# Kernel tuning notes

Hardware: AMD Instinct MI355X
Metric: run time of the kernel (lower is better)

The kernel has to match this reference:

```python
import jax, jax.numpy as jnp
import numpy as np

N_NODES = 100000
N_EDGES = 1600000
F_IN = 128
HID = 128
N_CLS = 7


def _sage_conv(x, src, dst, Wl, bl, Wr, n_nodes, deg_inv):
    # mean-aggregate neighbor messages at destination nodes
    msg = x[src]                                            # [E, d] gather
    agg = jax.ops.segment_sum(msg, dst, num_segments=n_nodes)
    agg = agg * deg_inv[:, None]                            # mean
    # PyG SAGEConv: lin_l(aggr) + lin_r(x); bias only on lin_l
    return agg @ Wl.T + bl + x @ Wr.T


def setup_inputs() -> dict:
    key = jax.random.key(0)
    ks = jax.random.split(key, 12)
    x = jax.random.normal(ks[0], (N_NODES, F_IN), dtype=jnp.float32)
    edge_index = jax.random.randint(ks[1], (2, N_EDGES), 0, N_NODES, dtype=jnp.int32)
    s = 0.05
    return {
        "x": x,
        "edge_index": edge_index,
        "W1l": jax.random.normal(ks[2], (HID, F_IN), dtype=jnp.float32) * s,
        "b1": jax.random.normal(ks[3], (HID,), dtype=jnp.float32) * s,
        "W1r": jax.random.normal(ks[4], (HID, F_IN), dtype=jnp.float32) * s,
        "W2l": jax.random.normal(ks[5], (HID, HID), dtype=jnp.float32) * s,
        "b2": jax.random.normal(ks[6], (HID,), dtype=jnp.float32) * s,
        "W2r": jax.random.normal(ks[7], (HID, HID), dtype=jnp.float32) * s,
        "W3l": jax.random.normal(ks[8], (N_CLS, HID), dtype=jnp.float32) * s,
        "b3": jax.random.normal(ks[9], (N_CLS,), dtype=jnp.float32) * s,
        "W3r": jax.random.normal(ks[10], (N_CLS, HID), dtype=jnp.float32) * s,
    }


def reference(x, edge_index, W1l, b1, W1r, W2l, b2, W2r, W3l, b3, W3r):
    src, dst = edge_index[0], edge_index[1]
    n = x.shape[0]
    # in-degree for mean aggregation (shared by all layers)
    deg = jax.ops.segment_sum(jnp.ones((src.shape[0],), x.dtype), dst, num_segments=n)
    deg_inv = jnp.where(deg > 0, 1.0 / deg, 0.0)

    h = _sage_conv(x, src, dst, W1l, b1, W1r, n, deg_inv)
    h = jax.nn.relu(h)  # dropout is identity in eval mode
    h = _sage_conv(h, src, dst, W2l, b2, W2r, n, deg_inv)
    h = jax.nn.relu(h)
    h = _sage_conv(h, src, dst, W3l, b3, W3r, n, deg_inv)
    return jax.nn.log_softmax(h, axis=1)
```

## Files before the change

kernel.cpp:

```cpp
#include <hip/hip_runtime.h>
#include <hip/hip_bf16.h>

#define NFEAT 128

typedef __attribute__((ext_vector_type(8))) short frag8;
typedef __attribute__((ext_vector_type(4))) float f32x4;

__device__ __forceinline__ unsigned short f2bf(float f) {
  unsigned int u = __builtin_bit_cast(unsigned int, f);
  u += 0x7fffu + ((u >> 16) & 1u);
  return (unsigned short)(u >> 16);
}
__device__ __forceinline__ unsigned int pack2(float lo, float hi) {
  return (unsigned int)f2bf(lo) | ((unsigned int)f2bf(hi) << 16);
}
__device__ __forceinline__ void acc_pair(float* acc, unsigned int u) {
  acc[0] += __builtin_bit_cast(float, u << 16);
  acc[1] += __builtin_bit_cast(float, u);
}
__device__ __forceinline__ void acc_uint4(float* a, const uint4& f) {
  acc_pair(a + 0, f.x);
  acc_pair(a + 2, f.y);
  acc_pair(a + 4, f.z);
  acc_pair(a + 6, f.w);
}

__global__ __launch_bounds__(256) void k_bucket_count(
    const int* __restrict__ dst, int* __restrict__ bucket_cnt, int E, int NB, int chunk) {
  __shared__ int hist[512];
  int t = threadIdx.x;
  hist[t] = 0;
  hist[t + 256] = 0;
  __syncthreads();
  int beg = blockIdx.x * chunk, end = min(beg + chunk, E);
  for (int i = beg + t; i < end; i += 256) atomicAdd(&hist[dst[i] >> 8], 1);
  __syncthreads();
  for (int k = t; k < NB; k += 256)
    if (hist[k]) atomicAdd(&bucket_cnt[k], hist[k]);
}

__global__ void k_bucket_scan(const int* __restrict__ bucket_cnt,
                              int* __restrict__ bucket_base,
                              int* __restrict__ bucket_cursor, int NB, int E) {
  __shared__ int sm[512];
  int t = threadIdx.x;
  int v = (t < NB) ? bucket_cnt[t] : 0;
  sm[t] = v;
  __syncthreads();
  for (int off = 1; off < 512; off <<= 1) {
    int add = (t >= off) ? sm[t - off] : 0;
    __syncthreads();
    sm[t] += add;
    __syncthreads();
  }
  int excl = sm[t] - v;
  if (t < NB) {
    bucket_base[t] = excl;
    bucket_cursor[t] = excl;
  }
  if (t == 0) bucket_base[NB] = E;
}

__global__ __launch_bounds__(256) void k_bucket_fill(
    const int* __restrict__ src, const int* __restrict__ dst,
    int* __restrict__ bucket_cursor, unsigned int* __restrict__ tmp,
    int E, int NB, int chunk) {
  __shared__ int hist[512];
  __shared__ int cur[512];
  int t = threadIdx.x;
  hist[t] = 0;
  hist[t + 256] = 0;
  __syncthreads();
  int beg = blockIdx.x * chunk, end = min(beg + chunk, E);
  for (int i = beg + t; i < end; i += 256) atomicAdd(&hist[dst[i] >> 8], 1);
  __syncthreads();
  for (int k = t; k < 512; k += 256)
    cur[k] = (k < NB && hist[k]) ? atomicAdd(&bucket_cursor[k], hist[k]) : 0;
  __syncthreads();
  for (int i = beg + t; i < end; i += 256) {
    int d = dst[i];
    int p = atomicAdd(&cur[d >> 8], 1);
    tmp[p] = (((unsigned int)(d & 255)) << 24) | (unsigned int)src[i];
  }
}

__global__ __launch_bounds__(256) void k_local_sort(
    const unsigned int* __restrict__ tmp, const int* __restrict__ bucket_base,
    int* __restrict__ csr, int* __restrict__ row_ptr, float* __restrict__ dinv,
    int N, int E) {
  __shared__ int cnt[256];
  __shared__ int scan_s[256];
  int b = blockIdx.x, t = threadIdx.x;
  int base = bucket_base[b];
  int cnt_b = bucket_base[b + 1] - base;
  cnt[t] = 0;
  __syncthreads();
  for (int i = t; i < cnt_b; i += 256) atomicAdd(&cnt[tmp[base + i] >> 24], 1);
  __syncthreads();
  int v = cnt[t];
  scan_s[t] = v;
  __syncthreads();
  for (int off = 1; off < 256; off <<= 1) {
    int add = (t >= off) ? scan_s[t - off] : 0;
    __syncthreads();
    scan_s[t] += add;
    __syncthreads();
  }
  int excl = scan_s[t] - v;
  int node = b * 256 + t;
  if (node <= N) row_ptr[node] = base + excl;
  if (node < N) dinv[node] = (v > 0) ? (1.0f / (float)v) : 0.0f;
  __syncthreads();
  cnt[t] = base + excl;
  __syncthreads();
  for (int i = t; i < cnt_b; i += 256) {
    unsigned int u = tmp[base + i];
    int q = atomicAdd(&cnt[u >> 24], 1);
    csr[q] = (int)(u & 0x00FFFFFFu);
  }
}

__global__ __launch_bounds__(256) void k_setup(
    const float* __restrict__ w1l, const float* __restrict__ w1r,
    const float* __restrict__ w2l, const float* __restrict__ w2r,
    const float* __restrict__ W3l, const float* __restrict__ W3r,
    unsigned short* __restrict__ Wbf, unsigned short* __restrict__ Wc,
    const float* __restrict__ x, unsigned int* __restrict__ Xbf,
    int n_pairs, int* __restrict__ bucket_cnt, int do_x) {
  int gid = blockIdx.x * 256 + threadIdx.x;
  int gstride = gridDim.x * 256;
  if (gid < 512) bucket_cnt[gid] = 0;
  if (gid < 65536) {
    int m = gid >> 14, off = gid & 16383;
    const float* srcw = (m == 0) ? w1l : (m == 1) ? w1r : (m == 2) ? w2l : w2r;
    Wbf[gid] = f2bf(srcw[off]);
  }
  if (gid < 2048) {
    int r = gid >> 7, c = gid & 127;
    float v = 0.f;
    if (r < 7) v = W3l[r * NFEAT + c];
    else if (r >= 8 && r < 15) v = W3r[(r - 8) * NFEAT + c];
    Wc[gid] = f2bf(v);
  }
  if (do_x) {
    for (int i = gid; i < n_pairs; i += gstride) {
      float2 v = *(const float2*)(x + (size_t)i * 2);
      Xbf[i] = pack2(v.x, v.y);
    }
  }
}

__global__ __launch_bounds__(256) void k_aggregate(
    const unsigned int* __restrict__ xp, const int* __restrict__ row_ptr,
    const int* __restrict__ csr, const float* __restrict__ dinv,
    unsigned int* __restrict__ Aout, int n) {
  int wv = threadIdx.x >> 6, lane = threadIdx.x & 63;
  int v = blockIdx.x * 4 + wv;
  if (v >= n) return;
  int beg = row_ptr[v], end = row_ptr[v + 1];
  float dv = dinv[v];
  int slot = lane >> 4, part = lane & 15;

  int idx = 0;
  if (beg + lane < end) idx = csr[beg + lane];

  float acc[8] = {0.f, 0.f, 0.f, 0.f, 0.f, 0.f, 0.f, 0.f};
  for (int j = beg; j < end; j += 16) {
    int sidx[4];
#pragma unroll
    for (int b = 0; b < 4; ++b) {
      int rel = (j - beg) + b * 4 + slot;
      sidx[b] = __shfl(idx, rel & 63);
    }
    uint4 f[4];
#pragma unroll
    for (int b = 0; b < 4; ++b) {
      f[b] = make_uint4(0u, 0u, 0u, 0u);
      int e = j + b * 4 + slot;
      if (e < end) {
        int rel = e - beg;
        int s = (rel < 64) ? sidx[b] : csr[e];
        f[b] = *(const uint4*)(xp + (size_t)s * (NFEAT / 2) + part * 4);
      }
    }
#pragma unroll
    for (int b = 0; b < 4; ++b) acc_uint4(acc, f[b]);
  }
#pragma unroll
  for (int k = 0; k < 8; ++k) {
    acc[k] += __shfl_xor(acc[k], 16);
    acc[k] += __shfl_xor(acc[k], 32);
  }
  if (slot == 0) {
    uint4 o;
    o.x = pack2(acc[0] * dv, acc[1] * dv);
    o.y = pack2(acc[2] * dv, acc[3] * dv);
    o.z = pack2(acc[4] * dv, acc[5] * dv);
    o.w = pack2(acc[6] * dv, acc[7] * dv);
    *(uint4*)(Aout + (size_t)v * (NFEAT / 2) + part * 4) = o;
  }
}

__global__ __launch_bounds__(256) void k_aggregate_f32(
    const float* __restrict__ xp, const int* __restrict__ row_ptr,
    const int* __restrict__ csr, const float* __restrict__ dinv,
    unsigned int* __restrict__ Aout, int n) {
  int wv = threadIdx.x >> 6, lane = threadIdx.x & 63;
  int v = blockIdx.x * 4 + wv;
  if (v >= n) return;
  int beg = row_ptr[v], end = row_ptr[v + 1];
  float dv = dinv[v];
  int slot = lane >> 5;
  int part = lane & 31;
  float acc[4] = {0.f, 0.f, 0.f, 0.f};
  for (int j = beg; j < end; j += 16) {
    float4 f[8];
#pragma unroll
    for (int b = 0; b < 8; ++b) {
      f[b] = make_float4(0.f, 0.f, 0.f, 0.f);
      int e = j + b * 2 + slot;
      if (e < end) {
        int si = csr[e];
        f[b] = *(const float4*)(xp + (size_t)si * NFEAT + part * 4);
      }
    }
#pragma unroll
    for (int b = 0; b < 8; ++b) {
      acc[0] += f[b].x; acc[1] += f[b].y; acc[2] += f[b].z; acc[3] += f[b].w;
    }
  }
#pragma unroll
  for (int k = 0; k < 4; ++k) acc[k] += __shfl_xor(acc[k], 32);
  if (slot == 0) {
    uint2 o;
    o.x = pack2(acc[0] * dv, acc[1] * dv);
    o.y = pack2(acc[2] * dv, acc[3] * dv);
    *(uint2*)(Aout + (size_t)v * (NFEAT / 2) + part * 2) = o;
  }
}

template <bool X_IS_F32, bool INPLACE>
__global__ __launch_bounds__(256, 4) void k_gemm(
    const unsigned short* __restrict__ A, const void* __restrict__ X,
    const unsigned short* __restrict__ Wl, const unsigned short* __restrict__ Wr,
    const float* __restrict__ bias, unsigned short* __restrict__ Out,
    int M, int ntiles) {
  int wv = threadIdx.x >> 6, lane = threadIdx.x & 63;
  int lr = lane & 15, kq = lane >> 4;
  int kb0 = kq * 8;

  frag8 wl[2][4], wr[2][4];
  float bias_c[2];
#pragma unroll
  for (int ci = 0; ci < 2; ++ci) {
    int wrow = (wv * 2 + ci) * 16 + lr;
    bias_c[ci] = bias[wrow];
#pragma unroll
    for (int kk = 0; kk < 4; ++kk) {
      wl[ci][kk] = *(const frag8*)(Wl + (size_t)wrow * NFEAT + kk * 32 + kb0);
      wr[ci][kk] = *(const frag8*)(Wr + (size_t)wrow * NFEAT + kk * 32 + kb0);
    }
  }

  for (int tile = blockIdx.x; tile < ntiles; tile += gridDim.x) {
    int m0 = tile * 16;
    int row = m0 + lr;
    bool rowok = row < M;
    frag8 aA[4], aX[4];
#pragma unroll
    for (int kk = 0; kk < 4; ++kk) {
      aA[kk] = frag8{};
      aX[kk] = frag8{};
      if (rowok) {
        aA[kk] = *(const frag8*)(A + (size_t)row * NFEAT + kk * 32 + kb0);
        if constexpr (X_IS_F32) {
          const float* xp = (const float*)X + (size_t)row * NFEAT + kk * 32 + kb0;
          float4 v0 = *(const float4*)xp;
          float4 v1 = *(const float4*)(xp + 4);
          frag8 a;
          a[0] = (short)f2bf(v0.x); a[1] = (short)f2bf(v0.y);
          a[2] = (short)f2bf(v0.z); a[3] = (short)f2bf(v0.w);
          a[4] = (short)f2bf(v1.x); a[5] = (short)f2bf(v1.y);
          a[6] = (short)f2bf(v1.z); a[7] = (short)f2bf(v1.w);
          aX[kk] = a;
        } else {
          aX[kk] = *(const frag8*)((const unsigned short*)X + (size_t)row * NFEAT + kk * 32 + kb0);
        }
      }
    }
    if constexpr (INPLACE) __syncthreads();
    f32x4 acc[2] = {};
#pragma unroll
    for (int kk = 0; kk < 4; ++kk) {
#pragma unroll
      for (int ci = 0; ci < 2; ++ci) {
        acc[ci] = __builtin_amdgcn_mfma_f32_16x16x32_bf16(aA[kk], wl[ci][kk], acc[ci], 0, 0, 0);
        acc[ci] = __builtin_amdgcn_mfma_f32_16x16x32_bf16(aX[kk], wr[ci][kk], acc[ci], 0, 0, 0);
      }
    }
#pragma unroll
    for (int ci = 0; ci < 2; ++ci) {
#pragma unroll
      for (int r = 0; r < 4; ++r) {
        int orow = m0 + kq * 4 + r;
        if (orow < M) {
          int ocol = (wv * 2 + ci) * 16 + lr;
          float val = acc[ci][r] + bias_c[ci];
          Out[(size_t)orow * NFEAT + ocol] = f2bf(fmaxf(val, 0.f));
        }
      }
    }
  }
}

__global__ __launch_bounds__(256) void k_proj7m(
    const unsigned short* __restrict__ H, const unsigned short* __restrict__ Wc,
    float* __restrict__ P, float* __restrict__ Q, int M, int ntiles) {
  int wv = threadIdx.x >> 6, lane = threadIdx.x & 63;
  int lr = lane & 15, kq = lane >> 4;
  int kb0 = kq * 8;
  frag8 wb[4];
#pragma unroll
  for (int kk = 0; kk < 4; ++kk)
    wb[kk] = *(const frag8*)(Wc + (size_t)lr * NFEAT + kk * 32 + kb0);

  int tile = blockIdx.x * 4 + wv;
  if (tile >= ntiles) return;
  int m0 = tile * 16;
  int row = m0 + lr;
  bool rowok = row < M;
  frag8 a[4];
#pragma unroll
  for (int kk = 0; kk < 4; ++kk) {
    a[kk] = frag8{};
    if (rowok) a[kk] = *(const frag8*)(H + (size_t)row * NFEAT + kk * 32 + kb0);
  }
  f32x4 acc = {};
#pragma unroll
  for (int kk = 0; kk < 4; ++kk)
    acc = __builtin_amdgcn_mfma_f32_16x16x32_bf16(a[kk], wb[kk], acc, 0, 0, 0);
#pragma unroll
  for (int r = 0; r < 4; ++r) {
    int orow = m0 + kq * 4 + r;
    if (orow < M) {
      if (lr < 8) P[(size_t)orow * 8 + lr] = acc[r];
      else Q[(size_t)orow * 8 + (lr - 8)] = acc[r];
    }
  }
}

__global__ __launch_bounds__(256) void k_layer3s(
    const float* __restrict__ P, const float* __restrict__ Q,
    const int* __restrict__ row_ptr, const int* __restrict__ csr,
    const float* __restrict__ dinv, const float* __restrict__ b3,
    float* __restrict__ out, int n) {
  int wv = threadIdx.x >> 6, lane = threadIdx.x & 63;
  int v = blockIdx.x * 4 + wv;
  if (v >= n) return;
  int beg = row_ptr[v], end = row_ptr[v + 1];
  int g = lane >> 3, c = lane & 7;
  float acc = 0.f;
  for (int j = beg; j < end; j += 16) {
    float f0 = 0.f, f1 = 0.f;
    int e0 = j + g, e1 = j + 8 + g;
    if (e0 < end) f0 = P[(size_t)csr[e0] * 8 + c];
    if (e1 < end) f1 = P[(size_t)csr[e1] * 8 + c];
    acc += f0 + f1;
  }
  acc += __shfl_xor(acc, 8);
  acc += __shfl_xor(acc, 16);
  acc += __shfl_xor(acc, 32);
  float z_own = acc * dinv[v] + Q[(size_t)v * 8 + c] + ((c < 7) ? b3[c] : 0.f);
  float mx = -1e30f, se = 0.f;
  float zz[7];
#pragma unroll
  for (int cc = 0; cc < 7; ++cc) {
    zz[cc] = __shfl(z_own, cc);
    mx = fmaxf(mx, zz[cc]);
  }
#pragma unroll
  for (int cc = 0; cc < 7; ++cc) se += __expf(zz[cc] - mx);
  float lse = mx + __logf(se);
  if (lane < 7) out[(size_t)v * 7 + lane] = z_own - lse;
}

extern "C" void kernel_launch(void* const* d_in, const int* in_sizes, int n_in,
                              void* d_out, int out_size, void* d_ws, size_t ws_size,
                              hipStream_t stream) {
  const float* x = (const float*)d_in[0];
  const int* ei = (const int*)d_in[1];
  const float* W1l = (const float*)d_in[2];
  const float* b1 = (const float*)d_in[3];
  const float* W1r = (const float*)d_in[4];
  const float* W2l = (const float*)d_in[5];
  const float* b2 = (const float*)d_in[6];
  const float* W2r = (const float*)d_in[7];
  const float* W3l = (const float*)d_in[8];
  const float* b3 = (const float*)d_in[9];
  const float* W3r = (const float*)d_in[10];
  float* out = (float*)d_out;

  int N = in_sizes[0] / NFEAT;
  int E = in_sizes[1] / 2;
  const int* src = ei;
  const int* dst = ei + E;

  char* ws = (char*)d_ws;
  size_t off = 0;
  auto alloc = [&](size_t bytes) {
    void* p = (void*)(ws + off);
    off += (bytes + 255) & ~(size_t)255;
    return p;
  };
  int* row_ptr = (int*)alloc((size_t)(N + 1) * 4);
  float* dinv = (float*)alloc((size_t)N * 4);
  int* bucket_cnt = (int*)alloc(512 * 4);
  int* bucket_base = (int*)alloc(513 * 4);
  int* bucket_cursor = (int*)alloc(512 * 4);
  int* csr = (int*)alloc((size_t)E * 4);
  unsigned short* Wbf = (unsigned short*)alloc((size_t)4 * 128 * 128 * 2);
  unsigned short* Wc = (unsigned short*)alloc((size_t)16 * 128 * 2);
  unsigned short* Abuf = (unsigned short*)alloc((size_t)N * NFEAT * 2);
  unsigned short* Bbuf = (unsigned short*)alloc((size_t)N * NFEAT * 2);
  size_t off_base = off;
  unsigned short* Xbf = (unsigned short*)alloc((size_t)N * NFEAT * 2);
  bool use_xbf = (off <= ws_size);
  if (!use_xbf) off = off_base;
  unsigned int* tmp = (unsigned int*)Abuf;
  float* P = (float*)Abuf;
  float* Q = P + (size_t)N * 8;

  int NB = (N + 255) >> 8;
  int chunk = (E + 255) / 256;
  int npairs = N * (NFEAT / 2);

  k_setup<<<2048, 256, 0, stream>>>(W1l, W1r, W2l, W2r, W3l, W3r, Wbf, Wc, x,
                                    (unsigned int*)Xbf, npairs, bucket_cnt,
                                    use_xbf ? 1 : 0);
  k_bucket_count<<<256, 256, 0, stream>>>(dst, bucket_cnt, E, NB, chunk);
  k_bucket_scan<<<1, 512, 0, stream>>>(bucket_cnt, bucket_base, bucket_cursor, NB, E);
  k_bucket_fill<<<256, 256, 0, stream>>>(src, dst, bucket_cursor, tmp, E, NB, chunk);
  k_local_sort<<<NB, 256, 0, stream>>>(tmp, bucket_base, csr, row_ptr, dinv, N, E);

  unsigned short* W1l_bf = Wbf;
  unsigned short* W1r_bf = Wbf + 16384;
  unsigned short* W2l_bf = Wbf + 32768;
  unsigned short* W2r_bf = Wbf + 49152;

  int gnode = (N + 3) / 4;
  int ntiles = (N + 15) / 16;
  int ggemm = min(ntiles, 1024);

  if (use_xbf) {
    k_aggregate<<<gnode, 256, 0, stream>>>((const unsigned int*)Xbf, row_ptr, csr, dinv,
                                           (unsigned int*)Abuf, N);
    k_gemm<false, false><<<ggemm, 256, 0, stream>>>(Abuf, Xbf, W1l_bf, W1r_bf, b1,
                                                    Bbuf, N, ntiles);
    k_aggregate<<<gnode, 256, 0, stream>>>((const unsigned int*)Bbuf, row_ptr, csr, dinv,
                                           (unsigned int*)Abuf, N);
    k_gemm<false, false><<<ggemm, 256, 0, stream>>>(Abuf, Bbuf, W2l_bf, W2r_bf, b2,
                                                    Xbf, N, ntiles);
    k_proj7m<<<(ntiles + 3) / 4, 256, 0, stream>>>(Xbf, Wc, P, Q, N, ntiles);
  } else {
    k_aggregate_f32<<<gnode, 256, 0, stream>>>(x, row_ptr, csr, dinv,
                                               (unsigned int*)Abuf, N);
    k_gemm<true, false><<<ggemm, 256, 0, stream>>>(Abuf, x, W1l_bf, W1r_bf, b1,
                                                   Bbuf, N, ntiles);
    k_aggregate<<<gnode, 256, 0, stream>>>((const unsigned int*)Bbuf, row_ptr, csr, dinv,
                                           (unsigned int*)Abuf, N);
    k_gemm<false, true><<<ggemm, 256, 0, stream>>>(Abuf, Bbuf, W2l_bf, W2r_bf, b2,
                                                   Bbuf, N, ntiles);
    k_proj7m<<<(ntiles + 3) / 4, 256, 0, stream>>>(Bbuf, Wc, P, Q, N, ntiles);
  }
  k_layer3s<<<gnode, 256, 0, stream>>>(P, Q, row_ptr, csr, dinv, b3, out, N);
}
```

Measured before the change: 301.1 us.

## Fuse neighbor aggregation with SAGE layer GEMM via shared-memory tile

```diff
diff --git a/kernel.cpp b/kernel.cpp
--- a/kernel.cpp
+++ b/kernel.cpp
@@ -2,6 +2,7 @@
 #include <hip/hip_bf16.h>
 
 #define NFEAT 128
+#define LPAD 136
 
 typedef __attribute__((ext_vector_type(8))) short frag8;
 typedef __attribute__((ext_vector_type(4))) float f32x4;
@@ -150,54 +151,111 @@
   }
 }
 
-__global__ __launch_bounds__(256) void k_aggregate(
-    const unsigned int* __restrict__ xp, const int* __restrict__ row_ptr,
+__global__ __launch_bounds__(256, 4) void k_agg_gemm(
+    const unsigned int* __restrict__ Hp,
+    const unsigned short* __restrict__ Wl, const unsigned short* __restrict__ Wr,
+    const float* __restrict__ bias, const int* __restrict__ row_ptr,
     const int* __restrict__ csr, const float* __restrict__ dinv,
-    unsigned int* __restrict__ Aout, int n) {
+    unsigned short* __restrict__ Out, int M, int ntiles) {
+  __shared__ unsigned short lds[16][LPAD];
   int wv = threadIdx.x >> 6, lane = threadIdx.x & 63;
-  int v = blockIdx.x * 4 + wv;
-  if (v >= n) return;
-  int beg = row_ptr[v], end = row_ptr[v + 1];
-  float dv = dinv[v];
-  int slot = lane >> 4, part = lane & 15;
-
-  int idx = 0;
-  if (beg + lane < end) idx = csr[beg + lane];
-
-  float acc[8] = {0.f, 0.f, 0.f, 0.f, 0.f, 0.f, 0.f, 0.f};
-  for (int j = beg; j < end; j += 16) {
-    int sidx[4];
-#pragma unroll
-    for (int b = 0; b < 4; ++b) {
-      int rel = (j - beg) + b * 4 + slot;
-      sidx[b] = __shfl(idx, rel & 63);
-    }
-    uint4 f[4];
-#pragma unroll
-    for (int b = 0; b < 4; ++b) {
-      f[b] = make_uint4(0u, 0u, 0u, 0u);
-      int e = j + b * 4 + slot;
-      if (e < end) {
-        int rel = e - beg;
-        int s = (rel < 64) ? sidx[b] : csr[e];
-        f[b] = *(const uint4*)(xp + (size_t)s * (NFEAT / 2) + part * 4);
-      }
-    }
-#pragma unroll
-    for (int b = 0; b < 4; ++b) acc_uint4(acc, f[b]);
-  }
-#pragma unroll
-  for (int k = 0; k < 8; ++k) {
-    acc[k] += __shfl_xor(acc[k], 16);
-    acc[k] += __shfl_xor(acc[k], 32);
-  }
-  if (slot == 0) {
-    uint4 o;
-    o.x = pack2(acc[0] * dv, acc[1] * dv);
-    o.y = pack2(acc[2] * dv, acc[3] * dv);
-    o.z = pack2(acc[4] * dv, acc[5] * dv);
-    o.w = pack2(acc[6] * dv, acc[7] * dv);
-    *(uint4*)(Aout + (size_t)v * (NFEAT / 2) + part * 4) = o;
+  int lr = lane & 15, kq = lane >> 4;
+  int kb0 = kq * 8;
+  int slot = kq, part = lr;
+
+  frag8 wl[2][4], wr[2][4];
+  float bias_c[2];
+#pragma unroll
+  for (int ci = 0; ci < 2; ++ci) {
+    int wrow = (wv * 2 + ci) * 16 + lr;
+    bias_c[ci] = bias[wrow];
+#pragma unroll
+    for (int kk = 0; kk < 4; ++kk) {
+      wl[ci][kk] = *(const frag8*)(Wl + (size_t)wrow * NFEAT + kk * 32 + kb0);
+      wr[ci][kk] = *(const frag8*)(Wr + (size_t)wrow * NFEAT + kk * 32 + kb0);
+    }
+  }
+
+  for (int tile = blockIdx.x; tile < ntiles; tile += gridDim.x) {
+    int m0 = tile * 16;
+#pragma unroll 1
+    for (int i = 0; i < 4; ++i) {
+      int v = m0 + wv * 4 + i;
+      if (v >= M) continue;
+      int beg = row_ptr[v], end = row_ptr[v + 1];
+      int idx = 0;
+      if (beg + lane < end) idx = csr[beg + lane];
+      float acc[8] = {0.f, 0.f, 0.f, 0.f, 0.f, 0.f, 0.f, 0.f};
+      for (int j = beg; j < end; j += 16) {
+        int sidx[4];
+#pragma unroll
+        for (int b = 0; b < 4; ++b) {
+          int rel = (j - beg) + b * 4 + slot;
+          sidx[b] = __shfl(idx, rel & 63);
+        }
+        uint4 f[4];
+#pragma unroll
+        for (int b = 0; b < 4; ++b) {
+          f[b] = make_uint4(0u, 0u, 0u, 0u);
+          int e = j + b * 4 + slot;
+          if (e < end) {
+            int rel = e - beg;
+            int s = (rel < 64) ? sidx[b] : csr[e];
+            f[b] = *(const uint4*)(Hp + (size_t)s * (NFEAT / 2) + part * 4);
+          }
+        }
+#pragma unroll
+        for (int b = 0; b < 4; ++b) acc_uint4(acc, f[b]);
+      }
+#pragma unroll
+      for (int k = 0; k < 8; ++k) {
+        acc[k] += __shfl_xor(acc[k], 16);
+        acc[k] += __shfl_xor(acc[k], 32);
+      }
+      if (slot == 0) {
+        float dv = dinv[v];
+        uint4 o;
+        o.x = pack2(acc[0] * dv, acc[1] * dv);
+        o.y = pack2(acc[2] * dv, acc[3] * dv);
+        o.z = pack2(acc[4] * dv, acc[5] * dv);
+        o.w = pack2(acc[6] * dv, acc[7] * dv);
+        *(uint4*)(&lds[wv * 4 + i][part * 8]) = o;
+      }
+    }
+    __syncthreads();
+    int row = m0 + lr;
+    bool rowok = row < M;
+    frag8 aA[4], aX[4];
+#pragma unroll
+    for (int kk = 0; kk < 4; ++kk) {
+      aA[kk] = *(const frag8*)(&lds[lr][kk * 32 + kb0]);
+      aX[kk] = frag8{};
+      if (rowok)
+        aX[kk] = *(const frag8*)((const unsigned short*)Hp + (size_t)row * NFEAT +
+                                 kk * 32 + kb0);
+    }
+    __syncthreads();
+    f32x4 acc2[2] = {};
+#pragma unroll
+    for (int kk = 0; kk < 4; ++kk) {
+#pragma unroll
+      for (int ci = 0; ci < 2; ++ci) {
+        acc2[ci] = __builtin_amdgcn_mfma_f32_16x16x32_bf16(aA[kk], wl[ci][kk], acc2[ci], 0, 0, 0);
+        acc2[ci] = __builtin_amdgcn_mfma_f32_16x16x32_bf16(aX[kk], wr[ci][kk], acc2[ci], 0, 0, 0);
+      }
+    }
+#pragma unroll
+    for (int ci = 0; ci < 2; ++ci) {
+#pragma unroll
+      for (int r = 0; r < 4; ++r) {
+        int orow = m0 + kq * 4 + r;
+        if (orow < M) {
+          int ocol = (wv * 2 + ci) * 16 + lr;
+          float val = acc2[ci][r] + bias_c[ci];
+          Out[(size_t)orow * NFEAT + ocol] = f2bf(fmaxf(val, 0.f));
+        }
+      }
+    }
   }
 }
 
@@ -239,6 +297,55 @@
   }
 }
 
+__global__ __launch_bounds__(256) void k_aggregate(
+    const unsigned int* __restrict__ xp, const int* __restrict__ row_ptr,
+    const int* __restrict__ csr, const float* __restrict__ dinv,
+    unsigned int* __restrict__ Aout, int n) {
+  int wv = threadIdx.x >> 6, lane = threadIdx.x & 63;
+  int v = blockIdx.x * 4 + wv;
+  if (v >= n) return;
+  int beg = row_ptr[v], end = row_ptr[v + 1];
+  float dv = dinv[v];
+  int slot = lane >> 4, part = lane & 15;
+  int idx = 0;
+  if (beg + lane < end) idx = csr[beg + lane];
+  float acc[8] = {0.f, 0.f, 0.f, 0.f, 0.f, 0.f, 0.f, 0.f};
+  for (int j = beg; j < end; j += 16) {
+    int sidx[4];
+#pragma unroll
+    for (int b = 0; b < 4; ++b) {
+      int rel = (j - beg) + b * 4 + slot;
+      sidx[b] = __shfl(idx, rel & 63);
+    }
+    uint4 f[4];
+#pragma unroll
+    for (int b = 0; b < 4; ++b) {
+      f[b] = make_uint4(0u, 0u, 0u, 0u);
+      int e = j + b * 4 + slot;
+      if (e < end) {
+        int rel = e - beg;
+        int s = (rel < 64) ? sidx[b] : csr[e];
+        f[b] = *(const uint4*)(xp + (size_t)s * (NFEAT / 2) + part * 4);
+      }
+    }
+#pragma unroll
+    for (int b = 0; b < 4; ++b) acc_uint4(acc, f[b]);
+  }
+#pragma unroll
+  for (int k = 0; k < 8; ++k) {
+    acc[k] += __shfl_xor(acc[k], 16);
+    acc[k] += __shfl_xor(acc[k], 32);
+  }
+  if (slot == 0) {
+    uint4 o;
+    o.x = pack2(acc[0] * dv, acc[1] * dv);
+    o.y = pack2(acc[2] * dv, acc[3] * dv);
+    o.z = pack2(acc[4] * dv, acc[5] * dv);
+    o.w = pack2(acc[6] * dv, acc[7] * dv);
+    *(uint4*)(Aout + (size_t)v * (NFEAT / 2) + part * 4) = o;
+  }
+}
+
 template <bool X_IS_F32, bool INPLACE>
 __global__ __launch_bounds__(256, 4) void k_gemm(
     const unsigned short* __restrict__ A, const void* __restrict__ X,
@@ -248,7 +355,6 @@
   int wv = threadIdx.x >> 6, lane = threadIdx.x & 63;
   int lr = lane & 15, kq = lane >> 4;
   int kb0 = kq * 8;
-
   frag8 wl[2][4], wr[2][4];
   float bias_c[2];
 #pragma unroll
@@ -261,7 +367,6 @@
       wr[ci][kk] = *(const frag8*)(Wr + (size_t)wrow * NFEAT + kk * 32 + kb0);
     }
   }
-
   for (int tile = blockIdx.x; tile < ntiles; tile += gridDim.x) {
     int m0 = tile * 16;
     int row = m0 + lr;
@@ -452,14 +557,10 @@
   int ggemm = min(ntiles, 1024);
 
   if (use_xbf) {
-    k_aggregate<<<gnode, 256, 0, stream>>>((const unsigned int*)Xbf, row_ptr, csr, dinv,
-                                           (unsigned int*)Abuf, N);
-    k_gemm<false, false><<<ggemm, 256, 0, stream>>>(Abuf, Xbf, W1l_bf, W1r_bf, b1,
-                                                    Bbuf, N, ntiles);
-    k_aggregate<<<gnode, 256, 0, stream>>>((const unsigned int*)Bbuf, row_ptr, csr, dinv,
-                                           (unsigned int*)Abuf, N);
-    k_gemm<false, false><<<ggemm, 256, 0, stream>>>(Abuf, Bbuf, W2l_bf, W2r_bf, b2,
-                                                    Xbf, N, ntiles);
+    k_agg_gemm<<<ggemm, 256, 0, stream>>>((const unsigned int*)Xbf, W1l_bf, W1r_bf, b1,
+                                          row_ptr, csr, dinv, Bbuf, N, ntiles);
+    k_agg_gemm<<<ggemm, 256, 0, stream>>>((const unsigned int*)Bbuf, W2l_bf, W2r_bf, b2,
+                                          row_ptr, csr, dinv, Xbf, N, ntiles);
     k_proj7m<<<(ntiles + 3) / 4, 256, 0, stream>>>(Xbf, Wc, P, Q, N, ntiles);
   } else {
     k_aggregate_f32<<<gnode, 256, 0, stream>>>(x, row_ptr, csr, dinv,
```

Result: slower. 340.1 us (+13.0%).
